# Performance work log

Hardware: AMD Instinct MI355X
Metric: run time of the kernel (lower is better)

The kernel has to match this reference:

```python
import jax, jax.numpy as jnp
import numpy as np

N_NODES = 100000
N_EDGES = 1600000
N_GRAPHS = 128
IN_F, H_F, OUT_F, HID, NCLS = 128, 128, 64, 10, 10

def setup_inputs() -> dict:
    key = jax.random.key(0)
    ks = jax.random.split(key, 12)
    feats = jax.random.normal(ks[0], (N_NODES, IN_F), dtype=jnp.float32)
    src = jax.random.randint(ks[1], (N_EDGES,), 0, N_NODES, dtype=jnp.int32)
    dst = jax.random.randint(ks[2], (N_EDGES,), 0, N_NODES, dtype=jnp.int32)
    graph_ids = jnp.sort(jax.random.randint(ks[3], (N_NODES,), 0, N_GRAPHS, dtype=jnp.int32))
    def glorot(k, shape):
        fan = shape[0] + shape[1]
        return jax.random.normal(k, shape, dtype=jnp.float32) * jnp.sqrt(2.0 / fan)
    return {
        'feats': feats, 'src': src, 'dst': dst, 'graph_ids': graph_ids,
        'W1': glorot(ks[4], (IN_F, H_F)), 'b1': jnp.zeros((H_F,), jnp.float32),
        'W2': glorot(ks[5], (H_F, OUT_F)), 'b2': jnp.zeros((OUT_F,), jnp.float32),
        'fcW1': glorot(ks[6], (OUT_F, HID)), 'fcb1': jnp.zeros((HID,), jnp.float32),
        'fcW2': glorot(ks[7], (HID, NCLS)), 'fcb2': jnp.zeros((NCLS,), jnp.float32),
    }

def _graph_conv(x, W, b, src, dst):
    # DGL GraphConv, norm='both': D_dst^{-1/2} A D_src^{-1/2} X W + b
    ones = jnp.ones((src.shape[0],), x.dtype)
    deg_out = jnp.clip(jax.ops.segment_sum(ones, src, num_segments=N_NODES), 1.0)
    deg_in = jnp.clip(jax.ops.segment_sum(ones, dst, num_segments=N_NODES), 1.0)
    x = x * jax.lax.rsqrt(deg_out)[:, None]
    m = jax.ops.segment_sum(x[src], dst, num_segments=N_NODES)  # gather-scatter over edges
    m = m * jax.lax.rsqrt(deg_in)[:, None]
    return m @ W + b

def reference(feats, src, dst, graph_ids, W1, b1, W2, b2, fcW1, fcb1, fcW2, fcb2):
    h = jax.nn.relu(_graph_conv(feats, W1, b1, src, dst))
    h = jax.nn.relu(_graph_conv(h, W2, b2, src, dst))
    # dgl.mean_nodes: per-graph mean pooling
    sums = jax.ops.segment_sum(h, graph_ids, num_segments=N_GRAPHS)
    counts = jnp.clip(jax.ops.segment_sum(jnp.ones((N_NODES,), h.dtype), graph_ids, num_segments=N_GRAPHS), 1.0)
    pooled = sums / counts[:, None]  # [G, OUT_F]
    z = jax.nn.relu(pooled @ fcW1 + fcb1)
    return jax.nn.softmax(z @ fcW2 + fcb2, axis=1)
```

## Files before the change

kernel.cpp:

```cpp
#include <hip/hip_runtime.h>
#include <hip/hip_bf16.h>

#define N_NODES 100000
#define N_EDGES 1600000
#define N_GRAPHS 128
#define IN_F 128
#define H_F 128
#define OUT_F 64
#define HID 10
#define NCLS 10
#define XPAD 136
#define BSH 7
#define NBUCK 782
#define SBLK 128
#define EPB (N_EDGES / SBLK)
#define NB_PREP 4
#define PCHUNK 8

typedef __attribute__((ext_vector_type(8))) short bf16x8;
typedef __attribute__((ext_vector_type(4))) float f32x4;
typedef __attribute__((ext_vector_type(2))) float f32x2;

__device__ __forceinline__ float bl(unsigned int u) { return __uint_as_float(u << 16); }
__device__ __forceinline__ float bh(unsigned int u) { return __uint_as_float(u & 0xffff0000u); }

__global__ __launch_bounds__(1024) void k_hist2(const int* __restrict__ src, const int* __restrict__ dst,
                                                int* __restrict__ Pd, int* __restrict__ Ps,
                                                const float* __restrict__ W1, const float* __restrict__ W2,
                                                unsigned short* __restrict__ Wt1, unsigned short* __restrict__ Wt2) {
    __shared__ int hd[NBUCK];
    __shared__ int hs[NBUCK];
    const int blk = blockIdx.x;
    if (blk < SBLK) {
        for (int i = threadIdx.x; i < NBUCK; i += 1024) { hd[i] = 0; hs[i] = 0; }
        __syncthreads();
        const int base = blk * EPB;
        for (int i = threadIdx.x; i < EPB; i += 1024) {
            atomicAdd(&hd[dst[base + i] >> BSH], 1);
            atomicAdd(&hs[src[base + i] >> BSH], 1);
        }
        __syncthreads();
        for (int b = threadIdx.x; b < NBUCK; b += 1024) {
            Pd[b * SBLK + blk] = hd[b];
            Ps[b * SBLK + blk] = hs[b];
        }
    } else {
        int t = (blk - SBLK) * 1024 + threadIdx.x;
        const int stride = NB_PREP * 1024;
        for (int i = t; i < 128 * 128; i += stride) {
            int c = i >> 7, k = i & 127;
            __hip_bfloat16 v = __float2bfloat16(W1[k * 128 + c]);
            Wt1[i] = *(unsigned short*)&v;
        }
        for (int i = t; i < 64 * 128; i += stride) {
            int c = i >> 7, k = i & 127;
            __hip_bfloat16 v = __float2bfloat16(W2[k * 64 + c]);
            Wt2[i] = *(unsigned short*)&v;
        }
    }
}

__global__ __launch_bounds__(128) void k_scanA(int* __restrict__ Pd, int* __restrict__ Ps,
                                               int* __restrict__ Td, int* __restrict__ Ts) {
    __shared__ int sc[128];
    const int b = blockIdx.x;
    const int t = threadIdx.x;
    int* P = (b < NBUCK) ? Pd : Ps;
    int* T = (b < NBUCK) ? Td : Ts;
    const int bb = (b < NBUCK) ? b : b - NBUCK;
    int v = P[bb * SBLK + t];
    sc[t] = v;
    __syncthreads();
    for (int off = 1; off < 128; off <<= 1) {
        int u = (t >= off) ? sc[t - off] : 0;
        __syncthreads();
        sc[t] += u;
        __syncthreads();
    }
    P[bb * SBLK + t] = sc[t] - v;
    if (t == 127) T[bb] = sc[127];
}

__global__ __launch_bounds__(1024) void k_scanB(const int* __restrict__ Td, const int* __restrict__ Ts,
                                                int* __restrict__ Bd, int* __restrict__ Bs) {
    __shared__ int sc[1024];
    const int t = threadIdx.x;
    int v = (t < NBUCK) ? Td[t] : 0;
    sc[t] = v;
    __syncthreads();
    for (int off = 1; off < 1024; off <<= 1) {
        int u = (t >= off) ? sc[t - off] : 0;
        __syncthreads();
        sc[t] += u;
        __syncthreads();
    }
    if (t < NBUCK) Bd[t] = sc[t] - v;
    if (t == NBUCK - 1) Bd[NBUCK] = sc[t];
    __syncthreads();
    int v2 = (t < NBUCK) ? Ts[t] : 0;
    sc[t] = v2;
    __syncthreads();
    for (int off = 1; off < 1024; off <<= 1) {
        int u = (t >= off) ? sc[t - off] : 0;
        __syncthreads();
        sc[t] += u;
        __syncthreads();
    }
    if (t < NBUCK) Bs[t] = sc[t] - v2;
    if (t == NBUCK - 1) Bs[NBUCK] = sc[t];
}

__global__ __launch_bounds__(1024) void k_scatter(const int* __restrict__ src, const int* __restrict__ dst,
                                                  const int* __restrict__ Pd, const int* __restrict__ Ps,
                                                  const int* __restrict__ Bd, const int* __restrict__ Bs,
                                                  unsigned int* __restrict__ pb, unsigned char* __restrict__ sb) {
    __shared__ int tk[NBUCK];
    const int b = blockIdx.x;
    const bool isPb = b < SBLK;
    const int blk = isPb ? b : b - SBLK;
    for (int i = threadIdx.x; i < NBUCK; i += 1024) tk[i] = 0;
    __syncthreads();
    const int base = blk * EPB;
    if (isPb) {
        for (int i = threadIdx.x; i < EPB; i += 1024) {
            int d = dst[base + i];
            int s = src[base + i];
            int bd = d >> BSH;
            int t = atomicAdd(&tk[bd], 1);
            pb[Bd[bd] + Pd[bd * SBLK + blk] + t] = ((unsigned)s << 7) | (unsigned)(d & 127);
        }
    } else {
        for (int i = threadIdx.x; i < EPB; i += 1024) {
            int s = src[base + i];
            int bs = s >> BSH;
            int t = atomicAdd(&tk[bs], 1);
            sb[Bs[bs] + Ps[bs * SBLK + blk] + t] = (unsigned char)(s & 127);
        }
    }
}

__global__ __launch_bounds__(256) void k_finalize(const unsigned int* __restrict__ pb, const int* __restrict__ Bd,
                                                  const unsigned char* __restrict__ sb, const int* __restrict__ Bs,
                                                  int* __restrict__ rp, int* __restrict__ cnt_out,
                                                  int* __restrict__ cols) {
    __shared__ int cnt[128];
    __shared__ int exc[128];
    __shared__ int tick[128];
    __shared__ int h[128];
    __shared__ int sc[128];
    const int b = blockIdx.x;
    const int tid = threadIdx.x;
    if (tid < 128) { cnt[tid] = 0; tick[tid] = 0; h[tid] = 0; }
    __syncthreads();
    const int e0 = Bd[b], e1 = Bd[b + 1];
    for (int i = e0 + tid; i < e1; i += 256) atomicAdd(&cnt[pb[i] & 127], 1);
    const int f0 = Bs[b], f1 = Bs[b + 1];
    for (int i = f0 + tid; i < f1; i += 256) atomicAdd(&h[sb[i]], 1);
    __syncthreads();
    if (tid < 128) sc[tid] = cnt[tid];
    __syncthreads();
    for (int off = 1; off < 128; off <<= 1) {
        int u = (tid < 128 && tid >= off) ? sc[tid - off] : 0;
        __syncthreads();
        if (tid < 128) sc[tid] += u;
        __syncthreads();
    }
    if (tid < 128) exc[tid] = sc[tid] - cnt[tid];
    __syncthreads();
    const int node0 = b << BSH;
    if (tid < 128 && node0 + tid < N_NODES) {
        rp[node0 + tid] = e0 + exc[tid];
        cnt_out[node0 + tid] = h[tid];
    }
    if (b == NBUCK - 1 && tid == 0) rp[N_NODES] = N_EDGES;
    for (int i = e0 + tid; i < e1; i += 256) {
        unsigned int p = pb[i];
        int loc = p & 127;
        int t = atomicAdd(&tick[loc], 1);
        cols[e0 + exc[loc] + t] = (int)(p >> 7);
    }
}

template <int TOTF, bool XBF16, bool OUT_FP8>
__global__ __launch_bounds__(256) void k_gemm_mfma(const void* __restrict__ Xv,
                                                   const unsigned short* __restrict__ Wt,
                                                   const int* __restrict__ cnt_out,
                                                   void* __restrict__ GoutV) {
    __shared__ __align__(16) unsigned short Xs[32 * XPAD];
    __shared__ __align__(16) unsigned short Ws[64 * XPAD];
    const int tid = threadIdx.x;
    const int cbase = blockIdx.y * 64;
    const int row0 = blockIdx.x * 32;

    if constexpr (XBF16) {
        const uint2* X2 = (const uint2*)Xv;
#pragma unroll
        for (int j = 0; j < 4; j++) {
            int i = tid + 256 * j;
            int r = i >> 5, kk = i & 31;
            uint2 u = X2[(size_t)(row0 + r) * 32 + kk];
            *(uint2*)&Xs[r * XPAD + kk * 4] = u;
        }
    } else {
        const float4* X4 = (const float4*)Xv;
#pragma unroll
        for (int j = 0; j < 4; j++) {
            int i = tid + 256 * j;
            int r = i >> 5, k4 = i & 31;
            float4 x = X4[(size_t)(row0 + r) * 32 + k4];
            __hip_bfloat162 lo = __float22bfloat162_rn({x.x, x.y});
            __hip_bfloat162 hi = __float22bfloat162_rn({x.z, x.w});
            uint2 u;
            u.x = *(unsigned int*)&lo;
            u.y = *(unsigned int*)&hi;
            *(uint2*)&Xs[r * XPAD + k4 * 4] = u;
        }
    }
    {
        const uint2* W2 = (const uint2*)Wt;
#pragma unroll
        for (int j = 0; j < 8; j++) {
            int i = tid + 256 * j;
            int c = i >> 5, kk = i & 31;
            uint2 u = W2[(size_t)(cbase + c) * 32 + kk];
            *(uint2*)&Ws[c * XPAD + kk * 4] = u;
        }
    }
    __syncthreads();

    const int lane = tid & 63;
    const int wv = tid >> 6;
    const int m = lane & 15;
    const int q = lane >> 4;
    const int roff = (wv & 1) * 16;
    const int coff = (wv >> 1) * 32;

    f32x4 acc0 = {0.f, 0.f, 0.f, 0.f}, acc1 = {0.f, 0.f, 0.f, 0.f};
#pragma unroll
    for (int ks = 0; ks < 4; ks++) {
        int kb = ks * 32 + q * 8;
        bf16x8 a  = *(const bf16x8*)&Xs[(roff + m) * XPAD + kb];
        bf16x8 b0 = *(const bf16x8*)&Ws[(coff + m) * XPAD + kb];
        bf16x8 b1 = *(const bf16x8*)&Ws[(coff + 16 + m) * XPAD + kb];
        acc0 = __builtin_amdgcn_mfma_f32_16x16x32_bf16(a, b0, acc0, 0, 0, 0);
        acc1 = __builtin_amdgcn_mfma_f32_16x16x32_bf16(a, b1, acc1, 0, 0, 0);
    }
#pragma unroll
    for (int r = 0; r < 4; r++) {
        int row = row0 + roff + q * 4 + r;
        float s = rsqrtf((float)max(cnt_out[row], 1));
        int col0 = cbase + coff + m;
        if constexpr (OUT_FP8) {
            unsigned int pk = __builtin_amdgcn_cvt_pk_fp8_f32(acc0[r] * s, acc1[r] * s, 0, false);
            unsigned char* gp = (unsigned char*)GoutV + (size_t)row * TOTF + col0;
            gp[0]  = (unsigned char)(pk & 0xffu);
            gp[16] = (unsigned char)((pk >> 8) & 0xffu);
        } else {
            unsigned short* Gout = (unsigned short*)GoutV;
            __hip_bfloat16 o0 = __float2bfloat16(acc0[r] * s);
            __hip_bfloat16 o1 = __float2bfloat16(acc1[r] * s);
            Gout[(size_t)row * TOTF + col0]      = *(unsigned short*)&o0;
            Gout[(size_t)row * TOTF + col0 + 16] = *(unsigned short*)&o1;
        }
    }
}

__global__ __launch_bounds__(256) void k_spmm128f8(const unsigned int* __restrict__ G,
                                                   const int* __restrict__ rp,
                                                   const int* __restrict__ cols,
                                                   const float* __restrict__ bias,
                                                   uint2* __restrict__ H2) {
    const int lane = threadIdx.x & 63;
    const int wave = threadIdx.x >> 6;
    const int v = blockIdx.x * 4 + wave;
    const int b0 = rp[v];
    const int deg = rp[v + 1] - b0;
    const int c = lane & 31;
    const int h = lane >> 5;
    float ax = 0.f, ay = 0.f, az = 0.f, aw = 0.f;
    for (int base = 0; base < deg; base += 64) {
        const int n = min(64, deg - base);
        const int mycol = (lane < n) ? cols[b0 + base + lane] : 0;
        const int n8 = n & ~7;
        for (int j = 0; j < n8; j += 8) {
            int s0 = __shfl(mycol, j + h);
            int s1 = __shfl(mycol, j + 2 + h);
            int s2 = __shfl(mycol, j + 4 + h);
            int s3 = __shfl(mycol, j + 6 + h);
            unsigned int u0 = G[(size_t)s0 * 32 + c];
            unsigned int u1 = G[(size_t)s1 * 32 + c];
            unsigned int u2 = G[(size_t)s2 * 32 + c];
            unsigned int u3 = G[(size_t)s3 * 32 + c];
            f32x2 l0 = __builtin_amdgcn_cvt_pk_f32_fp8(u0, false);
            f32x2 h0 = __builtin_amdgcn_cvt_pk_f32_fp8(u0, true);
            f32x2 l1 = __builtin_amdgcn_cvt_pk_f32_fp8(u1, false);
            f32x2 h1v = __builtin_amdgcn_cvt_pk_f32_fp8(u1, true);
            f32x2 l2 = __builtin_amdgcn_cvt_pk_f32_fp8(u2, false);
            f32x2 h2v = __builtin_amdgcn_cvt_pk_f32_fp8(u2, true);
            f32x2 l3 = __builtin_amdgcn_cvt_pk_f32_fp8(u3, false);
            f32x2 h3 = __builtin_amdgcn_cvt_pk_f32_fp8(u3, true);
            ax += (l0.x + l1.x) + (l2.x + l3.x);
            ay += (l0.y + l1.y) + (l2.y + l3.y);
            az += (h0.x + h1v.x) + (h2v.x + h3.x);
            aw += (h0.y + h1v.y) + (h2v.y + h3.y);
        }
        for (int j = n8; j < n; j += 2) {
            int idx = j + h;
            int sj = __shfl(mycol, min(idx, n - 1));
            if (idx < n) {
                unsigned int u = G[(size_t)sj * 32 + c];
                f32x2 lo = __builtin_amdgcn_cvt_pk_f32_fp8(u, false);
                f32x2 hi = __builtin_amdgcn_cvt_pk_f32_fp8(u, true);
                ax += lo.x; ay += lo.y; az += hi.x; aw += hi.y;
            }
        }
    }
    ax += __shfl_xor(ax, 32);
    ay += __shfl_xor(ay, 32);
    az += __shfl_xor(az, 32);
    aw += __shfl_xor(aw, 32);
    if (h == 0) {
        float r = rsqrtf((float)max(deg, 1));
        float4 b = *(const float4*)&bias[4 * c];
        __hip_bfloat162 p0 = __float22bfloat162_rn({fmaxf(fmaf(ax, r, b.x), 0.f),
                                                    fmaxf(fmaf(ay, r, b.y), 0.f)});
        __hip_bfloat162 p1 = __float22bfloat162_rn({fmaxf(fmaf(az, r, b.z), 0.f),
                                                    fmaxf(fmaf(aw, r, b.w), 0.f)});
        uint2 o;
        o.x = *(unsigned int*)&p0;
        o.y = *(unsigned int*)&p1;
        H2[(size_t)v * 32 + c] = o;
    }
}

__global__ __launch_bounds__(256) void k_spmm64f8(const unsigned int* __restrict__ G,
                                                  const int* __restrict__ rp,
                                                  const int* __restrict__ cols,
                                                  const float* __restrict__ bias,
                                                  uint2* __restrict__ H2) {
    const int lane = threadIdx.x & 63;
    const int wave = threadIdx.x >> 6;
    const int v = blockIdx.x * 4 + wave;
    const int b0 = rp[v];
    const int deg = rp[v + 1] - b0;
    const int c = lane & 15;
    const int h = lane >> 4;
    float ax = 0.f, ay = 0.f, az = 0.f, aw = 0.f;
    for (int base = 0; base < deg; base += 64) {
        const int n = min(64, deg - base);
        const int mycol = (lane < n) ? cols[b0 + base + lane] : 0;
        const int n16 = n & ~15;
        for (int j = 0; j < n16; j += 16) {
            int s0 = __shfl(mycol, j + h);
            int s1 = __shfl(mycol, j + 4 + h);
            int s2 = __shfl(mycol, j + 8 + h);
            int s3 = __shfl(mycol, j + 12 + h);
            unsigned int u0 = G[(size_t)s0 * 16 + c];
            unsigned int u1 = G[(size_t)s1 * 16 + c];
            unsigned int u2 = G[(size_t)s2 * 16 + c];
            unsigned int u3 = G[(size_t)s3 * 16 + c];
            f32x2 l0 = __builtin_amdgcn_cvt_pk_f32_fp8(u0, false);
            f32x2 h0 = __builtin_amdgcn_cvt_pk_f32_fp8(u0, true);
            f32x2 l1 = __builtin_amdgcn_cvt_pk_f32_fp8(u1, false);
            f32x2 h1v = __builtin_amdgcn_cvt_pk_f32_fp8(u1, true);
            f32x2 l2 = __builtin_amdgcn_cvt_pk_f32_fp8(u2, false);
            f32x2 h2v = __builtin_amdgcn_cvt_pk_f32_fp8(u2, true);
            f32x2 l3 = __builtin_amdgcn_cvt_pk_f32_fp8(u3, false);
            f32x2 h3 = __builtin_amdgcn_cvt_pk_f32_fp8(u3, true);
            ax += (l0.x + l1.x) + (l2.x + l3.x);
            ay += (l0.y + l1.y) + (l2.y + l3.y);
            az += (h0.x + h1v.x) + (h2v.x + h3.x);
            aw += (h0.y + h1v.y) + (h2v.y + h3.y);
        }
        for (int j = n16; j < n; j += 4) {
            int idx = j + h;
            int sj = __shfl(mycol, min(idx, n - 1));
            if (idx < n) {
                unsigned int u = G[(size_t)sj * 16 + c];
                f32x2 lo = __builtin_amdgcn_cvt_pk_f32_fp8(u, false);
                f32x2 hi = __builtin_amdgcn_cvt_pk_f32_fp8(u, true);
                ax += lo.x; ay += lo.y; az += hi.x; aw += hi.y;
            }
        }
    }
    ax += __shfl_xor(ax, 16); ax += __shfl_xor(ax, 32);
    ay += __shfl_xor(ay, 16); ay += __shfl_xor(ay, 32);
    az += __shfl_xor(az, 16); az += __shfl_xor(az, 32);
    aw += __shfl_xor(aw, 16); aw += __shfl_xor(aw, 32);
    if (h == 0) {
        float r = rsqrtf((float)max(deg, 1));
        float4 b = *(const float4*)&bias[4 * c];
        __hip_bfloat162 p0 = __float22bfloat162_rn({fmaxf(fmaf(ax, r, b.x), 0.f),
                                                    fmaxf(fmaf(ay, r, b.y), 0.f)});
        __hip_bfloat162 p1 = __float22bfloat162_rn({fmaxf(fmaf(az, r, b.z), 0.f),
                                                    fmaxf(fmaf(aw, r, b.w), 0.f)});
        uint2 o;
        o.x = *(unsigned int*)&p0;
        o.y = *(unsigned int*)&p1;
        H2[(size_t)v * 16 + c] = o;
    }
}

__global__ __launch_bounds__(256) void k_pool(const unsigned short* __restrict__ h2,
                                              const int* __restrict__ gid,
                                              float* __restrict__ part) {
    __shared__ int se[2];
    __shared__ float red[16][16][4];
    const int cpart = blockIdx.x;
    const int g = blockIdx.y;
    const int tid = threadIdx.x;
    if (tid < 2) {
        int target = g + tid;
        int lo = 0, hi = N_NODES;
        while (lo < hi) {
            int mid = (lo + hi) >> 1;
            if (gid[mid] < target) lo = mid + 1; else hi = mid;
        }
        se[tid] = lo;
    }
    __syncthreads();
    const int s = se[0], e = se[1];
    const int chunk = (e - s + PCHUNK - 1) / PCHUNK;
    const int lo = s + cpart * chunk;
    const int hi = min(lo + chunk, e);
    const int r = tid >> 4, cp = tid & 15;
    float a0 = 0.f, a1 = 0.f, a2 = 0.f, a3 = 0.f;
    const uint2* H = (const uint2*)h2;
    for (int v = lo + r; v < hi; v += 16) {
        uint2 u = H[(size_t)v * 16 + cp];
        a0 += bl(u.x); a1 += bh(u.x); a2 += bl(u.y); a3 += bh(u.y);
    }
    red[r][cp][0] = a0; red[r][cp][1] = a1; red[r][cp][2] = a2; red[r][cp][3] = a3;
    for (int off = 8; off > 0; off >>= 1) {
        __syncthreads();
        if (r < off) {
#pragma unroll
            for (int k = 0; k < 4; k++) red[r][cp][k] += red[r + off][cp][k];
        }
    }
    __syncthreads();
    if (r == 0) {
        float4 o = {red[0][cp][0], red[0][cp][1], red[0][cp][2], red[0][cp][3]};
        *(float4*)&part[((size_t)cpart * N_GRAPHS + g) * 64 + 4 * cp] = o;
    }
}

__global__ __launch_bounds__(64) void k_mlp(const float* __restrict__ part,
                                            const int* __restrict__ gid,
                                            const float* __restrict__ fcW1,
                                            const float* __restrict__ fcb1,
                                            const float* __restrict__ fcW2,
                                            const float* __restrict__ fcb2,
                                            float* __restrict__ out) {
    __shared__ int se[2];
    __shared__ float p[64];
    __shared__ float z[10];
    __shared__ float l[10];
    __shared__ float red[2];
    const int g = blockIdx.x;
    const int t = threadIdx.x;
    if (t < 2) {
        int target = g + t;
        int lo = 0, hi = N_NODES;
        while (lo < hi) {
            int mid = (lo + hi) >> 1;
            if (gid[mid] < target) lo = mid + 1; else hi = mid;
        }
        se[t] = lo;
    }
    __syncthreads();
    const int cnt = max(se[1] - se[0], 1);
    float a = 0.f;
#pragma unroll
    for (int c = 0; c < PCHUNK; c++) a += part[((size_t)c * N_GRAPHS + g) * 64 + t];
    p[t] = a / (float)cnt;
    __syncthreads();
    if (t < 10) {
        float acc = fcb1[t];
        for (int k = 0; k < 64; k++) acc = fmaf(p[k], fcW1[k * 10 + t], acc);
        z[t] = fmaxf(acc, 0.f);
    }
    __syncthreads();
    if (t < 10) {
        float acc = fcb2[t];
        for (int k = 0; k < 10; k++) acc = fmaf(z[k], fcW2[k * 10 + t], acc);
        l[t] = acc;
    }
    __syncthreads();
    if (t == 0) {
        float m = l[0];
        for (int i = 1; i < 10; i++) m = fmaxf(m, l[i]);
        float ssum = 0.f;
        for (int i = 0; i < 10; i++) ssum += expf(l[i] - m);
        red[0] = m;
        red[1] = ssum;
    }
    __syncthreads();
    if (t < 10) out[g * 10 + t] = expf(l[t] - red[0]) / red[1];
}

extern "C" void kernel_launch(void* const* d_in, const int* in_sizes, int n_in,
                              void* d_out, int out_size, void* d_ws, size_t ws_size,
                              hipStream_t stream) {
    const float* feats = (const float*)d_in[0];
    const int* src = (const int*)d_in[1];
    const int* dst = (const int*)d_in[2];
    const int* gid = (const int*)d_in[3];
    const float* W1 = (const float*)d_in[4];
    const float* b1 = (const float*)d_in[5];
    const float* W2 = (const float*)d_in[6];
    const float* b2 = (const float*)d_in[7];
    const float* fcW1 = (const float*)d_in[8];
    const float* fcb1 = (const float*)d_in[9];
    const float* fcW2 = (const float*)d_in[10];
    const float* fcb2 = (const float*)d_in[11];
    float* out = (float*)d_out;

    char* w = (char*)d_ws;
    size_t off = 0;
    auto alloc = [&](size_t bytes) -> void* {
        void* p = w + off;
        off = (off + bytes + 255) & ~(size_t)255;
        return p;
    };
    int* cnt_out = (int*)alloc(N_NODES * 4);
    int* rp      = (int*)alloc((N_NODES + 1) * 4);
    int* cols    = (int*)alloc((size_t)N_EDGES * 4);
    int* Pd      = (int*)alloc(NBUCK * SBLK * 4);
    int* Ps      = (int*)alloc(NBUCK * SBLK * 4);
    int* Td      = (int*)alloc(NBUCK * 4);
    int* Ts      = (int*)alloc(NBUCK * 4);
    int* Bd      = (int*)alloc((NBUCK + 1) * 4);
    int* Bs      = (int*)alloc((NBUCK + 1) * 4);
    unsigned int* pb  = (unsigned int*)alloc((size_t)N_EDGES * 4);
    unsigned char* sb = (unsigned char*)alloc((size_t)N_EDGES);
    unsigned short* Wt1 = (unsigned short*)alloc(128 * 128 * 2);
    unsigned short* Wt2 = (unsigned short*)alloc(64 * 128 * 2);
    unsigned char* g1 = (unsigned char*)alloc((size_t)N_NODES * 128);
    unsigned short* h1 = (unsigned short*)alloc((size_t)N_NODES * 128 * 2);
    unsigned char* g2 = (unsigned char*)alloc((size_t)N_NODES * 64);
    unsigned short* h2 = (unsigned short*)alloc((size_t)N_NODES * 64 * 2);
    float* part = (float*)alloc((size_t)PCHUNK * N_GRAPHS * 64 * 4);

    k_hist2<<<SBLK + NB_PREP, 1024, 0, stream>>>(src, dst, Pd, Ps, W1, W2, Wt1, Wt2);
    k_scanA<<<2 * NBUCK, 128, 0, stream>>>(Pd, Ps, Td, Ts);
    k_scanB<<<1, 1024, 0, stream>>>(Td, Ts, Bd, Bs);
    k_scatter<<<2 * SBLK, 1024, 0, stream>>>(src, dst, Pd, Ps, Bd, Bs, pb, sb);
    k_finalize<<<NBUCK, 256, 0, stream>>>(pb, Bd, sb, Bs, rp, cnt_out, cols);

    k_gemm_mfma<128, false, true><<<dim3(N_NODES / 32, 2), 256, 0, stream>>>(feats, Wt1, cnt_out, g1);
    k_spmm128f8<<<N_NODES / 4, 256, 0, stream>>>((const unsigned int*)g1, rp, cols, b1, (uint2*)h1);

    k_gemm_mfma<64, true, true><<<dim3(N_NODES / 32, 1), 256, 0, stream>>>(h1, Wt2, cnt_out, g2);
    k_spmm64f8<<<N_NODES / 4, 256, 0, stream>>>((const unsigned int*)g2, rp, cols, b2, (uint2*)h2);

    k_pool<<<dim3(PCHUNK, N_GRAPHS), 256, 0, stream>>>(h2, gid, part);
    k_mlp<<<N_GRAPHS, 64, 0, stream>>>(part, gid, fcW1, fcb1, fcW2, fcb2, out);
}
```

Before: 293.6 us.

## Compute full 128 columns per GEMM1 block and widen SpMM128 gathers to 8 bytes

Adds a dedicated layer-1 GEMM kernel in which each block computes all 128 output columns. Each fp32 feature row is therefore read and converted to bf16 once, where before it was read by two column blocks. The layer-1 SpMM now gathers 8 fp8 values per lane with 16 lanes per row, so four neighbors are fetched per instruction instead of two, and the result is written as 16-byte stores. Both SpMM kernels switch to packed f32x2 accumulators. The cost is more LDS per GEMM block, which can lower occupancy, and a longer shuffle reduction in the SpMM.

```diff
diff --git a/kernel.cpp b/kernel.cpp
--- a/kernel.cpp
+++ b/kernel.cpp
@@ -181,6 +181,79 @@
     }
 }
 
+__global__ __launch_bounds__(256) void k_gemm1(const float* __restrict__ X,
+                                               const unsigned short* __restrict__ Wt,
+                                               const int* __restrict__ cnt_out,
+                                               unsigned char* __restrict__ Gout) {
+    __shared__ __align__(16) unsigned short Xs[32 * XPAD];
+    __shared__ __align__(16) unsigned short Ws[128 * XPAD];
+    const int tid = threadIdx.x;
+    const int row0 = blockIdx.x * 32;
+
+    {
+        const float4* X4 = (const float4*)X;
+#pragma unroll
+        for (int j = 0; j < 4; j++) {
+            int i = tid + 256 * j;
+            int r = i >> 5, k4 = i & 31;
+            float4 x = X4[(size_t)(row0 + r) * 32 + k4];
+            __hip_bfloat162 lo = __float22bfloat162_rn({x.x, x.y});
+            __hip_bfloat162 hi = __float22bfloat162_rn({x.z, x.w});
+            uint2 u;
+            u.x = *(unsigned int*)&lo;
+            u.y = *(unsigned int*)&hi;
+            *(uint2*)&Xs[r * XPAD + k4 * 4] = u;
+        }
+    }
+    {
+        const uint2* W2 = (const uint2*)Wt;
+#pragma unroll
+        for (int j = 0; j < 16; j++) {
+            int i = tid + 256 * j;
+            int cc = i >> 5, kk = i & 31;
+            uint2 u = W2[(size_t)cc * 32 + kk];
+            *(uint2*)&Ws[cc * XPAD + kk * 4] = u;
+        }
+    }
+    __syncthreads();
+
+    const int lane = tid & 63;
+    const int wv = tid >> 6;
+    const int m = lane & 15;
+    const int q = lane >> 4;
+    const int cg = wv * 32;
+
+    f32x4 acc00 = {0.f, 0.f, 0.f, 0.f}, acc01 = {0.f, 0.f, 0.f, 0.f};
+    f32x4 acc10 = {0.f, 0.f, 0.f, 0.f}, acc11 = {0.f, 0.f, 0.f, 0.f};
+#pragma unroll
+    for (int ks = 0; ks < 4; ks++) {
+        int kb = ks * 32 + q * 8;
+        bf16x8 a0 = *(const bf16x8*)&Xs[m * XPAD + kb];
+        bf16x8 a1 = *(const bf16x8*)&Xs[(16 + m) * XPAD + kb];
+        bf16x8 b0 = *(const bf16x8*)&Ws[(cg + m) * XPAD + kb];
+        bf16x8 b1 = *(const bf16x8*)&Ws[(cg + 16 + m) * XPAD + kb];
+        acc00 = __builtin_amdgcn_mfma_f32_16x16x32_bf16(a0, b0, acc00, 0, 0, 0);
+        acc01 = __builtin_amdgcn_mfma_f32_16x16x32_bf16(a0, b1, acc01, 0, 0, 0);
+        acc10 = __builtin_amdgcn_mfma_f32_16x16x32_bf16(a1, b0, acc10, 0, 0, 0);
+        acc11 = __builtin_amdgcn_mfma_f32_16x16x32_bf16(a1, b1, acc11, 0, 0, 0);
+    }
+#pragma unroll
+    for (int r = 0; r < 4; r++) {
+        int rowA = row0 + q * 4 + r;
+        int rowB = rowA + 16;
+        float sA = rsqrtf((float)max(cnt_out[rowA], 1));
+        float sB = rsqrtf((float)max(cnt_out[rowB], 1));
+        unsigned int pkA = __builtin_amdgcn_cvt_pk_fp8_f32(acc00[r] * sA, acc01[r] * sA, 0, false);
+        unsigned int pkB = __builtin_amdgcn_cvt_pk_fp8_f32(acc10[r] * sB, acc11[r] * sB, 0, false);
+        unsigned char* gA = Gout + (size_t)rowA * 128 + cg + m;
+        gA[0]  = (unsigned char)(pkA & 0xffu);
+        gA[16] = (unsigned char)((pkA >> 8) & 0xffu);
+        unsigned char* gB = Gout + (size_t)rowB * 128 + cg + m;
+        gB[0]  = (unsigned char)(pkB & 0xffu);
+        gB[16] = (unsigned char)((pkB >> 8) & 0xffu);
+    }
+}
+
 template <int TOTF, bool XBF16, bool OUT_FP8>
 __global__ __launch_bounds__(256) void k_gemm_mfma(const void* __restrict__ Xv,
                                                    const unsigned short* __restrict__ Wt,
@@ -265,71 +338,79 @@
     }
 }
 
+__device__ __forceinline__ void acc8(uint2 u, f32x2& a01, f32x2& a23, f32x2& a45, f32x2& a67) {
+    a01 += __builtin_amdgcn_cvt_pk_f32_fp8(u.x, false);
+    a23 += __builtin_amdgcn_cvt_pk_f32_fp8(u.x, true);
+    a45 += __builtin_amdgcn_cvt_pk_f32_fp8(u.y, false);
+    a67 += __builtin_amdgcn_cvt_pk_f32_fp8(u.y, true);
+}
+__device__ __forceinline__ float red2(float x) {
+    x += __shfl_xor(x, 16);
+    x += __shfl_xor(x, 32);
+    return x;
+}
+
 __global__ __launch_bounds__(256) void k_spmm128f8(const unsigned int* __restrict__ G,
                                                    const int* __restrict__ rp,
                                                    const int* __restrict__ cols,
                                                    const float* __restrict__ bias,
-                                                   uint2* __restrict__ H2) {
+                                                   uint4* __restrict__ H4) {
     const int lane = threadIdx.x & 63;
     const int wave = threadIdx.x >> 6;
     const int v = blockIdx.x * 4 + wave;
     const int b0 = rp[v];
     const int deg = rp[v + 1] - b0;
-    const int c = lane & 31;
-    const int h = lane >> 5;
-    float ax = 0.f, ay = 0.f, az = 0.f, aw = 0.f;
+    const int c = lane & 15;
+    const int h = lane >> 4;
+    const uint2* G2 = (const uint2*)G;
+    f32x2 a01 = {0.f, 0.f}, a23 = {0.f, 0.f}, a45 = {0.f, 0.f}, a67 = {0.f, 0.f};
     for (int base = 0; base < deg; base += 64) {
         const int n = min(64, deg - base);
         const int mycol = (lane < n) ? cols[b0 + base + lane] : 0;
-        const int n8 = n & ~7;
-        for (int j = 0; j < n8; j += 8) {
+        const int n16 = n & ~15;
+        for (int j = 0; j < n16; j += 16) {
             int s0 = __shfl(mycol, j + h);
-            int s1 = __shfl(mycol, j + 2 + h);
-            int s2 = __shfl(mycol, j + 4 + h);
-            int s3 = __shfl(mycol, j + 6 + h);
-            unsigned int u0 = G[(size_t)s0 * 32 + c];
-            unsigned int u1 = G[(size_t)s1 * 32 + c];
-            unsigned int u2 = G[(size_t)s2 * 32 + c];
-            unsigned int u3 = G[(size_t)s3 * 32 + c];
-            f32x2 l0 = __builtin_amdgcn_cvt_pk_f32_fp8(u0, false);
-            f32x2 h0 = __builtin_amdgcn_cvt_pk_f32_fp8(u0, true);
-            f32x2 l1 = __builtin_amdgcn_cvt_pk_f32_fp8(u1, false);
-            f32x2 h1v = __builtin_amdgcn_cvt_pk_f32_fp8(u1, true);
-            f32x2 l2 = __builtin_amdgcn_cvt_pk_f32_fp8(u2, false);
-            f32x2 h2v = __builtin_amdgcn_cvt_pk_f32_fp8(u2, true);
-            f32x2 l3 = __builtin_amdgcn_cvt_pk_f32_fp8(u3, false);
-            f32x2 h3 = __builtin_amdgcn_cvt_pk_f32_fp8(u3, true);
-            ax += (l0.x + l1.x) + (l2.x + l3.x);
-            ay += (l0.y + l1.y) + (l2.y + l3.y);
-            az += (h0.x + h1v.x) + (h2v.x + h3.x);
-            aw += (h0.y + h1v.y) + (h2v.y + h3.y);
-        }
-        for (int j = n8; j < n; j += 2) {
+            int s1 = __shfl(mycol, j + 4 + h);
+            int s2 = __shfl(mycol, j + 8 + h);
+            int s3 = __shfl(mycol, j + 12 + h);
+            uint2 u0 = G2[(size_t)s0 * 16 + c];
+            uint2 u1 = G2[(size_t)s1 * 16 + c];
+            uint2 u2 = G2[(size_t)s2 * 16 + c];
+            uint2 u3 = G2[(size_t)s3 * 16 + c];
+            acc8(u0, a01, a23, a45, a67);
+            acc8(u1, a01, a23, a45, a67);
+            acc8(u2, a01, a23, a45, a67);
+            acc8(u3, a01, a23, a45, a67);
+        }
+        for (int j = n16; j < n; j += 4) {
             int idx = j + h;
             int sj = __shfl(mycol, min(idx, n - 1));
             if (idx < n) {
-                unsigned int u = G[(size_t)sj * 32 + c];
-                f32x2 lo = __builtin_amdgcn_cvt_pk_f32_fp8(u, false);
-                f32x2 hi = __builtin_amdgcn_cvt_pk_f32_fp8(u, true);
-                ax += lo.x; ay += lo.y; az += hi.x; aw += hi.y;
+                uint2 u = G2[(size_t)sj * 16 + c];
+                acc8(u, a01, a23, a45, a67);
             }
         }
     }
-    ax += __shfl_xor(ax, 32);
-    ay += __shfl_xor(ay, 32);
-    az += __shfl_xor(az, 32);
-    aw += __shfl_xor(aw, 32);
+    float r0 = red2(a01.x), r1 = red2(a01.y), r2 = red2(a23.x), r3 = red2(a23.y);
+    float r4 = red2(a45.x), r5 = red2(a45.y), r6 = red2(a67.x), r7 = red2(a67.y);
     if (h == 0) {
-        float r = rsqrtf((float)max(deg, 1));
-        float4 b = *(const float4*)&bias[4 * c];
-        __hip_bfloat162 p0 = __float22bfloat162_rn({fmaxf(fmaf(ax, r, b.x), 0.f),
-                                                    fmaxf(fmaf(ay, r, b.y), 0.f)});
-        __hip_bfloat162 p1 = __float22bfloat162_rn({fmaxf(fmaf(az, r, b.z), 0.f),
-                                                    fmaxf(fmaf(aw, r, b.w), 0.f)});
-        uint2 o;
+        float rs = rsqrtf((float)max(deg, 1));
+        float4 bA = *(const float4*)&bias[8 * c];
+        float4 bB = *(const float4*)&bias[8 * c + 4];
+        __hip_bfloat162 p0 = __float22bfloat162_rn({fmaxf(fmaf(r0, rs, bA.x), 0.f),
+                                                    fmaxf(fmaf(r1, rs, bA.y), 0.f)});
+        __hip_bfloat162 p1 = __float22bfloat162_rn({fmaxf(fmaf(r2, rs, bA.z), 0.f),
+                                                    fmaxf(fmaf(r3, rs, bA.w), 0.f)});
+        __hip_bfloat162 p2 = __float22bfloat162_rn({fmaxf(fmaf(r4, rs, bB.x), 0.f),
+                                                    fmaxf(fmaf(r5, rs, bB.y), 0.f)});
+        __hip_bfloat162 p3 = __float22bfloat162_rn({fmaxf(fmaf(r6, rs, bB.z), 0.f),
+                                                    fmaxf(fmaf(r7, rs, bB.w), 0.f)});
+        uint4 o;
         o.x = *(unsigned int*)&p0;
         o.y = *(unsigned int*)&p1;
-        H2[(size_t)v * 32 + c] = o;
+        o.z = *(unsigned int*)&p2;
+        o.w = *(unsigned int*)&p3;
+        H4[(size_t)v * 16 + c] = o;
     }
 }
 
@@ -345,7 +426,7 @@
     const int deg = rp[v + 1] - b0;
     const int c = lane & 15;
     const int h = lane >> 4;
-    float ax = 0.f, ay = 0.f, az = 0.f, aw = 0.f;
+    f32x2 a01 = {0.f, 0.f}, a23 = {0.f, 0.f};
     for (int base = 0; base < deg; base += 64) {
         const int n = min(64, deg - base);
         const int mycol = (lane < n) ? cols[b0 + base + lane] : 0;
@@ -359,34 +440,26 @@
             unsigned int u1 = G[(size_t)s1 * 16 + c];
             unsigned int u2 = G[(size_t)s2 * 16 + c];
             unsigned int u3 = G[(size_t)s3 * 16 + c];
-            f32x2 l0 = __builtin_amdgcn_cvt_pk_f32_fp8(u0, false);
-            f32x2 h0 = __builtin_amdgcn_cvt_pk_f32_fp8(u0, true);
-            f32x2 l1 = __builtin_amdgcn_cvt_pk_f32_fp8(u1, false);
-            f32x2 h1v = __builtin_amdgcn_cvt_pk_f32_fp8(u1, true);
-            f32x2 l2 = __builtin_amdgcn_cvt_pk_f32_fp8(u2, false);
-            f32x2 h2v = __builtin_amdgcn_cvt_pk_f32_fp8(u2, true);
-            f32x2 l3 = __builtin_amdgcn_cvt_pk_f32_fp8(u3, false);
-            f32x2 h3 = __builtin_amdgcn_cvt_pk_f32_fp8(u3, true);
-            ax += (l0.x + l1.x) + (l2.x + l3.x);
-            ay += (l0.y + l1.y) + (l2.y + l3.y);
-            az += (h0.x + h1v.x) + (h2v.x + h3.x);
-            aw += (h0.y + h1v.y) + (h2v.y + h3.y);
+            a01 += __builtin_amdgcn_cvt_pk_f32_fp8(u0, false);
+            a23 += __builtin_amdgcn_cvt_pk_f32_fp8(u0, true);
+            a01 += __builtin_amdgcn_cvt_pk_f32_fp8(u1, false);
+            a23 += __builtin_amdgcn_cvt_pk_f32_fp8(u1, true);
+            a01 += __builtin_amdgcn_cvt_pk_f32_fp8(u2, false);
+            a23 += __builtin_amdgcn_cvt_pk_f32_fp8(u2, true);
+            a01 += __builtin_amdgcn_cvt_pk_f32_fp8(u3, false);
+            a23 += __builtin_amdgcn_cvt_pk_f32_fp8(u3, true);
         }
         for (int j = n16; j < n; j += 4) {
             int idx = j + h;
             int sj = __shfl(mycol, min(idx, n - 1));
             if (idx < n) {
                 unsigned int u = G[(size_t)sj * 16 + c];
-                f32x2 lo = __builtin_amdgcn_cvt_pk_f32_fp8(u, false);
-                f32x2 hi = __builtin_amdgcn_cvt_pk_f32_fp8(u, true);
-                ax += lo.x; ay += lo.y; az += hi.x; aw += hi.y;
+                a01 += __builtin_amdgcn_cvt_pk_f32_fp8(u, false);
+                a23 += __builtin_amdgcn_cvt_pk_f32_fp8(u, true);
             }
         }
     }
-    ax += __shfl_xor(ax, 16); ax += __shfl_xor(ax, 32);
-    ay += __shfl_xor(ay, 16); ay += __shfl_xor(ay, 32);
-    az += __shfl_xor(az, 16); az += __shfl_xor(az, 32);
-    aw += __shfl_xor(aw, 16); aw += __shfl_xor(aw, 32);
+    float ax = red2(a01.x), ay = red2(a01.y), az = red2(a23.x), aw = red2(a23.y);
     if (h == 0) {
         float r = rsqrtf((float)max(deg, 1));
         float4 b = *(const float4*)&bias[4 * c];
@@ -548,8 +621,8 @@
     k_scatter<<<2 * SBLK, 1024, 0, stream>>>(src, dst, Pd, Ps, Bd, Bs, pb, sb);
     k_finalize<<<NBUCK, 256, 0, stream>>>(pb, Bd, sb, Bs, rp, cnt_out, cols);
 
-    k_gemm_mfma<128, false, true><<<dim3(N_NODES / 32, 2), 256, 0, stream>>>(feats, Wt1, cnt_out, g1);
-    k_spmm128f8<<<N_NODES / 4, 256, 0, stream>>>((const unsigned int*)g1, rp, cols, b1, (uint2*)h1);
+    k_gemm1<<<N_NODES / 32, 256, 0, stream>>>(feats, Wt1, cnt_out, g1);
+    k_spmm128f8<<<N_NODES / 4, 256, 0, stream>>>((const unsigned int*)g1, rp, cols, b1, (uint4*)h1);
 
     k_gemm_mfma<64, true, true><<<dim3(N_NODES / 32, 1), 256, 0, stream>>>(h1, Wt2, cnt_out, g2);
     k_spmm64f8<<<N_NODES / 4, 256, 0, stream>>>((const unsigned int*)g2, rp, cols, b2, (uint2*)h2);
```

New measurement: 287.9 us. About the same (-1.9%).
